# Kernel optimization log

Measured on AMD Instinct MI355X. Metric: run time of the kernel, lower is better.

Reference implementation:

```python
import jax, jax.numpy as jnp
import numpy as np

NEG = -9.0e15

def gat_layer(X, adj_mask, W, Wb, a1, a2, ab):
    # X: [N, Fin]; W: [Fin, Fout]; a1,a2: [Fout]; ab: scalar
    h = X @ W + Wb                                   # [N, Fout]
    # a([h_i || h_j]) = h_i@a1 + h_j@a2 + ab  (decomposition of concat+linear)
    e = jax.nn.leaky_relu((h @ a1)[:, None] + (h @ a2)[None, :] + ab,
                          negative_slope=0.2)        # [N, N]
    e = jnp.where(adj_mask, e, NEG)
    attn = jax.nn.softmax(e, axis=1)                 # [N, N]
    return jax.nn.elu(attn @ h)                      # [N, Fout]

def setup_inputs() -> dict:
    key = jax.random.key(0)
    ks = jax.random.split(key, 12)
    N, Fin, Fh, H, Fout = 4096, 512, 128, 4, 64
    X = jax.random.normal(ks[0], (N, Fin), dtype=jnp.float32)
    adjacency_matrix = jax.random.randint(ks[1], (N, N), 0, 2, dtype=jnp.int32)
    s_in = 1.0 / np.sqrt(Fin)
    s_a = 1.0 / np.sqrt(2 * Fh)
    W_h  = jax.random.uniform(ks[2], (H, Fin, Fh), jnp.float32, -s_in, s_in)
    b_h  = jax.random.uniform(ks[3], (H, Fh), jnp.float32, -s_in, s_in)
    a1_h = jax.random.uniform(ks[4], (H, Fh), jnp.float32, -s_a, s_a)
    a2_h = jax.random.uniform(ks[5], (H, Fh), jnp.float32, -s_a, s_a)
    ab_h = jax.random.uniform(ks[6], (H,), jnp.float32, -s_a, s_a)
    Fcat = H * Fh
    s_c = 1.0 / np.sqrt(Fcat)
    s_ao = 1.0 / np.sqrt(2 * Fout)
    W_o  = jax.random.uniform(ks[7], (Fcat, Fout), jnp.float32, -s_c, s_c)
    b_o  = jax.random.uniform(ks[8], (Fout,), jnp.float32, -s_c, s_c)
    a1_o = jax.random.uniform(ks[9], (Fout,), jnp.float32, -s_ao, s_ao)
    a2_o = jax.random.uniform(ks[10], (Fout,), jnp.float32, -s_ao, s_ao)
    ab_o = jax.random.uniform(ks[11], (), jnp.float32, -s_ao, s_ao)
    return {"X": X, "adjacency_matrix": adjacency_matrix,
            "W_h": W_h, "b_h": b_h, "a1_h": a1_h, "a2_h": a2_h, "ab_h": ab_h,
            "W_o": W_o, "b_o": b_o, "a1_o": a1_o, "a2_o": a2_o, "ab_o": ab_o}

def reference(X, adjacency_matrix, W_h, b_h, a1_h, a2_h, ab_h,
              W_o, b_o, a1_o, a2_o, ab_o):
    adj_mask = adjacency_matrix > 0
    # per-head attention layers, vmapped over heads
    heads = jax.vmap(gat_layer, in_axes=(None, None, 0, 0, 0, 0, 0))(
        X, adj_mask, W_h, b_h, a1_h, a2_h, ab_h)      # [H, N, Fh]
    H, N, Fh = heads.shape
    x = jnp.transpose(heads, (1, 0, 2)).reshape(N, H * Fh)  # concat along features
    x = gat_layer(x, adj_mask, W_o, b_o, a1_o, a2_o, ab_o)  # [N, Fout]
    return jax.nn.log_softmax(x, axis=1)
```

## Files before the change

### kernel.cpp

```cpp
#include <hip/hip_runtime.h>
#include <math.h>

#define NN 4096
#define LOG2E 1.44269504088896340736f

using f32x4  = __attribute__((ext_vector_type(4))) float;
using bf16x4 = __attribute__((ext_vector_type(4))) __bf16;
using bf16x8 = __attribute__((ext_vector_type(8))) __bf16;

#if __has_builtin(__builtin_amdgcn_exp2f)
#define EXP2(x) __builtin_amdgcn_exp2f(x)
#else
#define EXP2(x) __expf((x) * 0.6931471805599453f)
#endif

#define WAITVM4_BARRIER asm volatile("s_waitcnt vmcnt(4)\ns_barrier" ::: "memory")
#define WAITVM0_BARRIER asm volatile("s_waitcnt vmcnt(0)\ns_barrier" ::: "memory")

template<int FH>
__device__ __forceinline__ void stage_tile(const __bf16* __restrict__ hgp,
                                           __bf16* dst, int tid) {
#pragma unroll
    for (int it = 0; it < FH / 32; it++) {
        int c = tid + it * 256;
        int f = c >> 3, sl = c & 7;
        int g = sl ^ (f & 7);
        __builtin_amdgcn_global_load_lds(
            (const __attribute__((address_space(1))) void*)(hgp + (size_t)f * NN + g * 8),
            (__attribute__((address_space(3))) void*)(dst + (size_t)c * 8), 16, 0, 0);
    }
}

__device__ __forceinline__ void stage_g(const __bf16* __restrict__ base, int ldk,
                                        __bf16* dst, int tid) {
#pragma unroll
    for (int it = 0; it < 2; it++) {
        int c = tid + it * 256;
        int f = c >> 3, sl = c & 7;
        int g = sl ^ (f & 7);
        __builtin_amdgcn_global_load_lds(
            (const __attribute__((address_space(1))) void*)(base + (size_t)f * ldk + g * 8),
            (__attribute__((address_space(3))) void*)(dst + (size_t)c * 8), 16, 0, 0);
    }
}

__global__ void prep_kernel(const int* __restrict__ adj, unsigned long long* __restrict__ bits,
                            const float* __restrict__ W_h, const float* __restrict__ b_h,
                            const float* __restrict__ W_o,
                            __bf16* __restrict__ Bt1, float* __restrict__ biasp,
                            __bf16* __restrict__ Bt2,
                            const float* __restrict__ X, __bf16* __restrict__ Xb,
                            float* __restrict__ zeros) {
    const int b = blockIdx.x, t = threadIdx.x;
    if (b < 1024) {
        int idx = b * 256 + t;
        {
            int n = idx >> 9, k = idx & 511;
            int h = n >> 7, f = n & 127;
            Bt1[idx] = (__bf16)W_h[(size_t)h * 512 * 128 + k * 128 + f];
        }
        if (idx < 64 * 512) {
            int n = idx >> 9, k = idx & 511;
            Bt2[idx] = (__bf16)W_o[k * 64 + n];
        }
        if (idx < 512) biasp[idx] = b_h[idx];
        if (idx < (10 * NN) / 4)
            *(f32x4*)(zeros + (size_t)idx * 4) = (f32x4){0.f, 0.f, 0.f, 0.f};
    } else if (b < 3072) {
        int i = (b - 1024) * 256 + t;
        f32x4 v = *(const f32x4*)(X + (size_t)i * 4);
        bf16x4 o;
#pragma unroll
        for (int q = 0; q < 4; q++) o[q] = (__bf16)v[q];
        *(bf16x4*)(Xb + (size_t)i * 4) = o;
    } else {
        int wave = (b - 3072) * 4 + (t >> 6);
        int lane = t & 63;
        int g0 = wave * 16;
        for (int it = 0; it < 16; it++) {
            int gw = g0 + it;
            int v = adj[(size_t)gw * 64 + lane];
            unsigned long long m = __ballot(v > 0);
            if (lane == 0) bits[gw] = m;
        }
    }
}

__global__ __launch_bounds__(256) void gemm_fused_kernel(
    const __bf16* __restrict__ A, const __bf16* __restrict__ Bt,
    const float* __restrict__ bias,
    const float* __restrict__ a1, const float* __restrict__ a2,
    __bf16* __restrict__ Ht, float* __restrict__ s1, float* __restrict__ s2,
    int M, int N, int K)
{
    __shared__ __attribute__((aligned(16))) __bf16 As[3][64 * 64];
    __shared__ __attribute__((aligned(16))) __bf16 Bs[3][64 * 64];
    const int tid = threadIdx.x, w = tid >> 6, l = tid & 63, o = l >> 4, rl = l & 15;
    const int bm = blockIdx.y * 64, bn = blockIdx.x * 64;
    f32x4 acc[4] = {};
    stage_g(A + (size_t)bm * K, K, &As[0][0], tid);
    stage_g(Bt + (size_t)bn * K, K, &Bs[0][0], tid);
    stage_g(A + (size_t)bm * K + 64, K, &As[1][0], tid);
    stage_g(Bt + (size_t)bn * K + 64, K, &Bs[1][0], tid);
    const int KB = K / 64;
    int b = 0;
    for (int kb = 0; kb < KB; kb++) {
        if (kb + 1 < KB) { WAITVM4_BARRIER; }
        else             { WAITVM0_BARRIER; }
#pragma unroll
        for (int kt = 0; kt < 2; kt++) {
            int ra = w * 16 + rl;
            int cg = kt * 4 + o;
            bf16x8 af = *(const bf16x8*)(&As[b][(ra * 8 + (cg ^ (ra & 7))) * 8]);
#pragma unroll
            for (int nt = 0; nt < 4; nt++) {
                int rb = nt * 16 + rl;
                bf16x8 bfr = *(const bf16x8*)(&Bs[b][(rb * 8 + (cg ^ (rb & 7))) * 8]);
                acc[nt] = __builtin_amdgcn_mfma_f32_16x16x32_bf16(af, bfr, acc[nt], 0, 0, 0);
            }
        }
        if (kb + 2 < KB) {
            int b2 = b + 2; if (b2 >= 3) b2 -= 3;
            stage_g(A + (size_t)bm * K + (kb + 2) * 64, K, &As[b2][0], tid);
            stage_g(Bt + (size_t)bn * K + (kb + 2) * 64, K, &Bs[b2][0], tid);
        }
        if (++b == 3) b = 0;
    }
    const int head = bn >> 7;
    const int row_base = bm + w * 16 + o * 4;
    float p1[4] = {0.f, 0.f, 0.f, 0.f}, p2[4] = {0.f, 0.f, 0.f, 0.f};
#pragma unroll
    for (int nt = 0; nt < 4; nt++) {
        int col = bn + nt * 16 + rl;
        float bv = bias[col];
        float a1v = a1[col] * LOG2E, a2v = a2[col] * LOG2E;
        bf16x4 hv;
#pragma unroll
        for (int r4 = 0; r4 < 4; r4++) {
            float h = acc[nt][r4] + bv;
            hv[r4] = (__bf16)h;
            p1[r4] += h * a1v;
            p2[r4] += h * a2v;
        }
        *(bf16x4*)(Ht + (size_t)col * M + row_base) = hv;
    }
#pragma unroll
    for (int r4 = 0; r4 < 4; r4++)
#pragma unroll
        for (int off = 1; off < 16; off <<= 1) {
            p1[r4] += __shfl_xor(p1[r4], off, 64);
            p2[r4] += __shfl_xor(p2[r4], off, 64);
        }
    if (rl == 0)
#pragma unroll
        for (int r4 = 0; r4 < 4; r4++) {
            atomicAdd(&s1[(size_t)head * M + row_base + r4], p1[r4]);
            atomicAdd(&s2[(size_t)head * M + row_base + r4], p2[r4]);
        }
}

template<int FH, int JSPLIT>
__global__ __launch_bounds__(256, 4) void attn_kernel(
    const __bf16* __restrict__ Htg,
    const unsigned long long* __restrict__ adj_bits,
    const float* __restrict__ s1_all, const float* __restrict__ s2_all,
    const float* __restrict__ ab_all,
    __bf16* __restrict__ accp,
    float* __restrict__ lg,
    int ldo)
{
    constexpr int NJT = NN / 64 / JSPLIT;
    constexpr int NTL = FH / 16;
    const int head = blockIdx.y;
    const int js   = blockIdx.z;
    const int row0 = blockIdx.x * 64;
    const int jt0  = js * NJT;
    const int tid = threadIdx.x;
    const int w = tid >> 6, l = tid & 63, o = l >> 4, rl = l & 15;
    const int myrow = row0 + w * 16 + rl;

    __shared__ __attribute__((aligned(16))) __bf16 hbuf[2][FH * 64];

    const float* s2 = s2_all + (size_t)head * NN;
    const __bf16* hg = Htg + (size_t)head * FH * NN;
    const float s1r = s1_all[(size_t)head * NN + myrow] + ab_all[head] * LOG2E;
    const float u0 = s1r;
    const float v0 = 0.2f * s1r;
    float lacc = 0.f;
    f32x4 acc[NTL] = {};

    unsigned long long aw;
    f32x4 sA0, sB0, sA1, sB1;

    auto PLOAD = [&](int jt) {
        aw = adj_bits[(size_t)myrow * 64 + jt];
        const float* sp = s2 + jt * 64 + o * 8;
        sA0 = *(const f32x4*)(sp);       sB0 = *(const f32x4*)(sp + 4);
        sA1 = *(const f32x4*)(sp + 32);  sB1 = *(const f32x4*)(sp + 36);
    };
    auto PMATH = [&](bf16x8& f0, bf16x8& f1) {
        float ps = 0.f;
        {
            unsigned int mb = (unsigned int)(aw >> (o * 8)) & 0xFFu;
#pragma unroll
            for (int q = 0; q < 8; q++) {
                float s = (q < 4) ? sA0[q] : sB0[q - 4];
                float t = fmaxf(s + u0, fmaf(0.2f, s, v0));
                t = ((mb >> q) & 1u) ? t : -1.0e20f;
                float p = EXP2(t);
                f0[q] = (__bf16)p; ps += p;
            }
        }
        {
            unsigned int mb = (unsigned int)(aw >> (32 + o * 8)) & 0xFFu;
#pragma unroll
            for (int q = 0; q < 8; q++) {
                float s = (q < 4) ? sA1[q] : sB1[q - 4];
                float t = fmaxf(s + u0, fmaf(0.2f, s, v0));
                t = ((mb >> q) & 1u) ? t : -1.0e20f;
                float p = EXP2(t);
                f1[q] = (__bf16)p; ps += p;
            }
        }
        lacc += ps;
    };

    stage_tile<FH>(hg + (size_t)jt0 * 64, &hbuf[0][0], tid);
    PLOAD(jt0);
    bf16x8 fc0, fc1, fn0, fn1;
    PMATH(fc0, fc1);
    if (NJT > 1) PLOAD(jt0 + 1);

    for (int jl = 0; jl < NJT; jl++) {
        const int b = jl & 1;
        const int jt = jt0 + jl;
        __syncthreads();
        if (jl + 1 < NJT)
            stage_tile<FH>(hg + (size_t)(jt + 1) * 64, &hbuf[b ^ 1][0], tid);
        __builtin_amdgcn_s_setprio(1);
        if (jl + 1 < NJT) PMATH(fn0, fn1);
        if (jl + 2 < NJT) PLOAD(jt + 2);
#pragma unroll
        for (int ntl = 0; ntl < NTL; ntl++) {
            int f = ntl * 16 + rl;
            int s0 = o ^ (rl & 7);
            int s1 = (4 + o) ^ (rl & 7);
            bf16x8 b0 = *(const bf16x8*)(&hbuf[b][(f * 8 + s0) * 8]);
            bf16x8 b1 = *(const bf16x8*)(&hbuf[b][(f * 8 + s1) * 8]);
            acc[ntl] = __builtin_amdgcn_mfma_f32_16x16x32_bf16(fc0, b0, acc[ntl], 0, 0, 0);
            acc[ntl] = __builtin_amdgcn_mfma_f32_16x16x32_bf16(fc1, b1, acc[ntl], 0, 0, 0);
        }
        __builtin_amdgcn_s_setprio(0);
        if (jl + 1 < NJT) { fc0 = fn0; fc1 = fn1; }
    }
    lacc += __shfl_xor(lacc, 16, 64);
    lacc += __shfl_xor(lacc, 32, 64);
    if (l < 16) lg[((size_t)head * JSPLIT + js) * NN + row0 + w * 16 + l] = lacc;
#pragma unroll
    for (int ntl = 0; ntl < NTL; ntl++)
#pragma unroll
        for (int r4 = 0; r4 < 4; r4++) {
            int grow = row0 + w * 16 + o * 4 + r4;
            int gcol = head * FH + ntl * 16 + rl;
            accp[((size_t)js * NN + grow) * ldo + gcol] = (__bf16)acc[ntl][r4];
        }
}

__global__ void combine1_kernel(const __bf16* __restrict__ accp, const float* __restrict__ lg,
                                __bf16* __restrict__ outb) {
    int gid = blockIdx.x * 256 + threadIdx.x;
    int row = gid >> 7, c4 = (gid & 127) * 4;
    int head = c4 >> 7;
    float lsum = 0.f;
#pragma unroll
    for (int js = 0; js < 4; js++) lsum += lg[((size_t)head * 4 + js) * NN + row];
    float inv = lsum > 0.f ? 1.f / lsum : 0.f;
    float v[4] = {0.f, 0.f, 0.f, 0.f};
#pragma unroll
    for (int js = 0; js < 4; js++) {
        bf16x4 t = *(const bf16x4*)(accp + ((size_t)js * NN + row) * 512 + c4);
#pragma unroll
        for (int q = 0; q < 4; q++) v[q] += (float)t[q];
    }
    bf16x4 ob;
#pragma unroll
    for (int q = 0; q < 4; q++) {
        float x = v[q] * inv;
        x = x > 0.f ? x : __expf(x) - 1.f;
        ob[q] = (__bf16)x;
    }
    *(bf16x4*)(outb + (size_t)row * 512 + c4) = ob;
}

__global__ void combine2_kernel(const __bf16* __restrict__ accp, const float* __restrict__ lg,
                                float* __restrict__ out) {
    int row = (blockIdx.x * 256 + threadIdx.x) >> 6;
    int lane = threadIdx.x & 63;
    if (row >= NN) return;
    float lsum = 0.f, v = 0.f;
#pragma unroll
    for (int js = 0; js < 16; js++) {
        lsum += lg[(size_t)js * NN + row];
        v += (float)accp[((size_t)js * NN + row) * 64 + lane];
    }
    float inv = lsum > 0.f ? 1.f / lsum : 0.f;
    v *= inv;
    v = v > 0.f ? v : __expf(v) - 1.f;
    float m = v;
#pragma unroll
    for (int off = 1; off < 64; off <<= 1) m = fmaxf(m, __shfl_xor(m, off, 64));
    float ex = __expf(v - m);
    float s = ex;
#pragma unroll
    for (int off = 1; off < 64; off <<= 1) s += __shfl_xor(s, off, 64);
    out[(size_t)row * 64 + lane] = v - m - __logf(s);
}

extern "C" void kernel_launch(void* const* d_in, const int* in_sizes, int n_in,
                              void* d_out, int out_size, void* d_ws, size_t ws_size,
                              hipStream_t stream) {
    const float* X    = (const float*)d_in[0];
    const int*   adj  = (const int*)d_in[1];
    const float* W_h  = (const float*)d_in[2];
    const float* b_h  = (const float*)d_in[3];
    const float* a1_h = (const float*)d_in[4];
    const float* a2_h = (const float*)d_in[5];
    const float* ab_h = (const float*)d_in[6];
    const float* W_o  = (const float*)d_in[7];
    const float* b_o  = (const float*)d_in[8];
    const float* a1_o = (const float*)d_in[9];
    const float* a2_o = (const float*)d_in[10];
    const float* ab_o = (const float*)d_in[11];
    float* out = (float*)d_out;

    char* ws = (char*)d_ws;
    auto alloc = [&](size_t bytes) {
        char* p = ws; ws += (bytes + 255) & ~(size_t)255; return p;
    };
    unsigned long long* adj_bits = (unsigned long long*)alloc((size_t)NN * 64 * 8);
    __bf16* Bt1    = (__bf16*)alloc((size_t)512 * 512 * 2);
    float*  biasp  = (float*)alloc(512 * 4);
    __bf16* Bt2    = (__bf16*)alloc((size_t)64 * 512 * 2);
    __bf16* Xb     = (__bf16*)alloc((size_t)NN * 512 * 2);
    float*  s1h    = (float*)alloc((size_t)4 * NN * 4);
    float*  s2h    = (float*)alloc((size_t)4 * NN * 4);
    float*  s1o    = (float*)alloc((size_t)NN * 4);
    float*  s2o    = (float*)alloc((size_t)NN * 4);
    __bf16* Htg    = (__bf16*)alloc((size_t)512 * NN * 2);
    __bf16* accp1  = (__bf16*)alloc((size_t)4 * NN * 512 * 2);
    float*  lg1    = (float*)alloc((size_t)16 * NN * 4);
    __bf16* outhb  = (__bf16*)alloc((size_t)NN * 512 * 2);
    __bf16* Ht2    = (__bf16*)alloc((size_t)64 * NN * 2);
    __bf16* accp2  = (__bf16*)alloc((size_t)16 * NN * 64 * 2);
    float*  lg2    = (float*)alloc((size_t)16 * NN * 4);

    prep_kernel<<<7168, 256, 0, stream>>>(adj, adj_bits, W_h, b_h, W_o,
                                          Bt1, biasp, Bt2, X, Xb, s1h);
    gemm_fused_kernel<<<dim3(8, 64), 256, 0, stream>>>(
        Xb, Bt1, biasp, a1_h, a2_h, Htg, s1h, s2h, NN, 512, 512);
    attn_kernel<128, 4><<<dim3(NN / 64, 4, 4), 256, 0, stream>>>(
        Htg, adj_bits, s1h, s2h, ab_h, accp1, lg1, 512);
    combine1_kernel<<<(NN * 128) / 256, 256, 0, stream>>>(accp1, lg1, outhb);
    gemm_fused_kernel<<<dim3(1, 64), 256, 0, stream>>>(
        outhb, Bt2, b_o, a1_o, a2_o, Ht2, s1o, s2o, NN, 64, 512);
    attn_kernel<64, 16><<<dim3(NN / 64, 1, 16), 256, 0, stream>>>(
        Ht2, adj_bits, s1o, s2o, ab_o, accp2, lg2, 64);
    combine2_kernel<<<(NN * 64) / 256, 256, 0, stream>>>(accp2, lg2, out);
}
```

Before: 204.1 us.

## Move adjacency bitpacking into first GEMM launch as extra z-slice blocks

Adjacency bit-packing moves out of the prep kernel and into 512 extra blocks (blockIdx.z==1) of the first fused GEMM launch. That lets the memory-bound 64MB int adjacency read run alongside the compute-bound GEMM instead of serially in prep. Each of these waves now packs 128 words instead of 16, so fewer blocks do the work with longer loops. Separately, the s_setprio(1) in the attention kernel now comes after the softmax math and prefetch, so only the MFMA section runs at raised priority.

```diff
diff --git a/kernel.cpp b/kernel.cpp
--- a/kernel.cpp
+++ b/kernel.cpp
@@ -44,8 +44,7 @@
     }
 }
 
-__global__ void prep_kernel(const int* __restrict__ adj, unsigned long long* __restrict__ bits,
-                            const float* __restrict__ W_h, const float* __restrict__ b_h,
+__global__ void prep_kernel(const float* __restrict__ W_h, const float* __restrict__ b_h,
                             const float* __restrict__ W_o,
                             __bf16* __restrict__ Bt1, float* __restrict__ biasp,
                             __bf16* __restrict__ Bt2,
@@ -66,23 +65,13 @@
         if (idx < 512) biasp[idx] = b_h[idx];
         if (idx < (10 * NN) / 4)
             *(f32x4*)(zeros + (size_t)idx * 4) = (f32x4){0.f, 0.f, 0.f, 0.f};
-    } else if (b < 3072) {
+    } else {
         int i = (b - 1024) * 256 + t;
         f32x4 v = *(const f32x4*)(X + (size_t)i * 4);
         bf16x4 o;
 #pragma unroll
         for (int q = 0; q < 4; q++) o[q] = (__bf16)v[q];
         *(bf16x4*)(Xb + (size_t)i * 4) = o;
-    } else {
-        int wave = (b - 3072) * 4 + (t >> 6);
-        int lane = t & 63;
-        int g0 = wave * 16;
-        for (int it = 0; it < 16; it++) {
-            int gw = g0 + it;
-            int v = adj[(size_t)gw * 64 + lane];
-            unsigned long long m = __ballot(v > 0);
-            if (lane == 0) bits[gw] = m;
-        }
     }
 }
 
@@ -91,11 +80,23 @@
     const float* __restrict__ bias,
     const float* __restrict__ a1, const float* __restrict__ a2,
     __bf16* __restrict__ Ht, float* __restrict__ s1, float* __restrict__ s2,
+    const int* __restrict__ adj, unsigned long long* __restrict__ adj_bits,
     int M, int N, int K)
 {
     __shared__ __attribute__((aligned(16))) __bf16 As[3][64 * 64];
     __shared__ __attribute__((aligned(16))) __bf16 Bs[3][64 * 64];
     const int tid = threadIdx.x, w = tid >> 6, l = tid & 63, o = l >> 4, rl = l & 15;
+    if (blockIdx.z == 1) {
+        int bid = blockIdx.y * gridDim.x + blockIdx.x;
+        int wv = bid * 4 + w;
+        for (int it = 0; it < 128; it++) {
+            int gw = wv * 128 + it;
+            int v = adj[(size_t)gw * 64 + l];
+            unsigned long long m = __ballot(v > 0);
+            if (l == 0) adj_bits[gw] = m;
+        }
+        return;
+    }
     const int bm = blockIdx.y * 64, bn = blockIdx.x * 64;
     f32x4 acc[4] = {};
     stage_g(A + (size_t)bm * K, K, &As[0][0], tid);
@@ -237,9 +238,9 @@
         __syncthreads();
         if (jl + 1 < NJT)
             stage_tile<FH>(hg + (size_t)(jt + 1) * 64, &hbuf[b ^ 1][0], tid);
-        __builtin_amdgcn_s_setprio(1);
         if (jl + 1 < NJT) PMATH(fn0, fn1);
         if (jl + 2 < NJT) PLOAD(jt + 2);
+        __builtin_amdgcn_s_setprio(1);
 #pragma unroll
         for (int ntl = 0; ntl < NTL; ntl++) {
             int f = ntl * 16 + rl;
@@ -354,15 +355,14 @@
     __bf16* accp2  = (__bf16*)alloc((size_t)16 * NN * 64 * 2);
     float*  lg2    = (float*)alloc((size_t)16 * NN * 4);
 
-    prep_kernel<<<7168, 256, 0, stream>>>(adj, adj_bits, W_h, b_h, W_o,
-                                          Bt1, biasp, Bt2, X, Xb, s1h);
-    gemm_fused_kernel<<<dim3(8, 64), 256, 0, stream>>>(
-        Xb, Bt1, biasp, a1_h, a2_h, Htg, s1h, s2h, NN, 512, 512);
+    prep_kernel<<<3072, 256, 0, stream>>>(W_h, b_h, W_o, Bt1, biasp, Bt2, X, Xb, s1h);
+    gemm_fused_kernel<<<dim3(8, 64, 2), 256, 0, stream>>>(
+        Xb, Bt1, biasp, a1_h, a2_h, Htg, s1h, s2h, adj, adj_bits, NN, 512, 512);
     attn_kernel<128, 4><<<dim3(NN / 64, 4, 4), 256, 0, stream>>>(
         Htg, adj_bits, s1h, s2h, ab_h, accp1, lg1, 512);
     combine1_kernel<<<(NN * 128) / 256, 256, 0, stream>>>(accp1, lg1, outhb);
-    gemm_fused_kernel<<<dim3(1, 64), 256, 0, stream>>>(
-        outhb, Bt2, b_o, a1_o, a2_o, Ht2, s1o, s2o, NN, 64, 512);
+    gemm_fused_kernel<<<dim3(1, 64, 1), 256, 0, stream>>>(
+        outhb, Bt2, b_o, a1_o, a2_o, Ht2, s1o, s2o, adj, adj_bits, NN, 64, 512);
     attn_kernel<64, 16><<<dim3(NN / 64, 1, 16), 256, 0, stream>>>(
         Ht2, adj_bits, s1o, s2o, ab_o, accp2, lg2, 64);
     combine2_kernel<<<(NN * 64) / 256, 256, 0, stream>>>(accp2, lg2, out);
```

Result: slower. 247.9 us (+21.4%).

## Fuse head-combine normalization and ELU into second-layer GEMM A-operand staging

Applied to the files above, without the earlier changes.

Drops the separate combine1 kernel. The second-layer GEMM now builds its A tiles directly from the split attention partials: it sums the 4 splits, scales by the reciprocal softmax denominators cached in shared memory, applies ELU, and writes swizzled bf16 into LDS. This removes one launch and the write and re-read of the 4096x512 intermediate. In exchange, the fused path uses double buffering with synchronous register-staged loads and only 64 blocks, so load latency may sit exposed in that GEMM. It also moves the s_setprio raise in the attention loop to after the softmax math and prefetch issue.

```diff
diff --git a/kernel.cpp b/kernel.cpp
--- a/kernel.cpp
+++ b/kernel.cpp
@@ -86,45 +86,109 @@
     }
 }
 
+template<int FUSEA>
 __global__ __launch_bounds__(256) void gemm_fused_kernel(
     const __bf16* __restrict__ A, const __bf16* __restrict__ Bt,
     const float* __restrict__ bias,
     const float* __restrict__ a1, const float* __restrict__ a2,
     __bf16* __restrict__ Ht, float* __restrict__ s1, float* __restrict__ s2,
+    const __bf16* __restrict__ accp, const float* __restrict__ lgin,
     int M, int N, int K)
 {
-    __shared__ __attribute__((aligned(16))) __bf16 As[3][64 * 64];
-    __shared__ __attribute__((aligned(16))) __bf16 Bs[3][64 * 64];
+    constexpr int NB = FUSEA ? 2 : 3;
+    __shared__ __attribute__((aligned(16))) __bf16 As[NB][64 * 64];
+    __shared__ __attribute__((aligned(16))) __bf16 Bs[NB][64 * 64];
+    __shared__ float sinv[4][64];
     const int tid = threadIdx.x, w = tid >> 6, l = tid & 63, o = l >> 4, rl = l & 15;
     const int bm = blockIdx.y * 64, bn = blockIdx.x * 64;
     f32x4 acc[4] = {};
-    stage_g(A + (size_t)bm * K, K, &As[0][0], tid);
-    stage_g(Bt + (size_t)bn * K, K, &Bs[0][0], tid);
-    stage_g(A + (size_t)bm * K + 64, K, &As[1][0], tid);
-    stage_g(Bt + (size_t)bn * K + 64, K, &Bs[1][0], tid);
     const int KB = K / 64;
-    int b = 0;
-    for (int kb = 0; kb < KB; kb++) {
-        if (kb + 1 < KB) { WAITVM4_BARRIER; }
-        else             { WAITVM0_BARRIER; }
-#pragma unroll
-        for (int kt = 0; kt < 2; kt++) {
-            int ra = w * 16 + rl;
-            int cg = kt * 4 + o;
-            bf16x8 af = *(const bf16x8*)(&As[b][(ra * 8 + (cg ^ (ra & 7))) * 8]);
-#pragma unroll
-            for (int nt = 0; nt < 4; nt++) {
-                int rb = nt * 16 + rl;
-                bf16x8 bfr = *(const bf16x8*)(&Bs[b][(rb * 8 + (cg ^ (rb & 7))) * 8]);
-                acc[nt] = __builtin_amdgcn_mfma_f32_16x16x32_bf16(af, bfr, acc[nt], 0, 0, 0);
-            }
-        }
-        if (kb + 2 < KB) {
-            int b2 = b + 2; if (b2 >= 3) b2 -= 3;
-            stage_g(A + (size_t)bm * K + (kb + 2) * 64, K, &As[b2][0], tid);
-            stage_g(Bt + (size_t)bn * K + (kb + 2) * 64, K, &Bs[b2][0], tid);
-        }
-        if (++b == 3) b = 0;
+
+    auto stageA_fused = [&](int kb, __bf16* dst) {
+#pragma unroll
+        for (int it = 0; it < 2; it++) {
+            int c = tid + it * 256;
+            int f = c >> 3, sl = c & 7;
+            int row = bm + f;
+            int col = kb * 64 + sl * 8;
+            float inv = sinv[kb >> 1][f];
+            float vs[8] = {0.f, 0.f, 0.f, 0.f, 0.f, 0.f, 0.f, 0.f};
+#pragma unroll
+            for (int js = 0; js < 4; js++) {
+                bf16x8 t = *(const bf16x8*)(accp + ((size_t)js * NN + row) * 512 + col);
+#pragma unroll
+                for (int q = 0; q < 8; q++) vs[q] += (float)t[q];
+            }
+            bf16x8 ob;
+#pragma unroll
+            for (int q = 0; q < 8; q++) {
+                float x = vs[q] * inv;
+                x = x > 0.f ? x : __expf(x) - 1.f;
+                ob[q] = (__bf16)x;
+            }
+            *(bf16x8*)(dst + ((size_t)f * 8 + (sl ^ (f & 7))) * 8) = ob;
+        }
+    };
+
+    if constexpr (FUSEA) {
+        {
+            int h = tid >> 6, r = tid & 63;
+            float ls = 0.f;
+#pragma unroll
+            for (int js = 0; js < 4; js++) ls += lgin[((size_t)(h * 4 + js)) * NN + bm + r];
+            sinv[h][r] = ls > 0.f ? 1.f / ls : 0.f;
+        }
+        __syncthreads();
+        stageA_fused(0, &As[0][0]);
+        stage_g(Bt + (size_t)bn * K, K, &Bs[0][0], tid);
+        for (int kb = 0; kb < KB; kb++) {
+            int b = kb & 1;
+            __syncthreads();
+            if (kb + 1 < KB) {
+                stageA_fused(kb + 1, &As[b ^ 1][0]);
+                stage_g(Bt + (size_t)bn * K + (kb + 1) * 64, K, &Bs[b ^ 1][0], tid);
+            }
+#pragma unroll
+            for (int kt = 0; kt < 2; kt++) {
+                int ra = w * 16 + rl;
+                int cg = kt * 4 + o;
+                bf16x8 af = *(const bf16x8*)(&As[b][(ra * 8 + (cg ^ (ra & 7))) * 8]);
+#pragma unroll
+                for (int nt = 0; nt < 4; nt++) {
+                    int rb = nt * 16 + rl;
+                    bf16x8 bfr = *(const bf16x8*)(&Bs[b][(rb * 8 + (cg ^ (rb & 7))) * 8]);
+                    acc[nt] = __builtin_amdgcn_mfma_f32_16x16x32_bf16(af, bfr, acc[nt], 0, 0, 0);
+                }
+            }
+        }
+    } else {
+        stage_g(A + (size_t)bm * K, K, &As[0][0], tid);
+        stage_g(Bt + (size_t)bn * K, K, &Bs[0][0], tid);
+        stage_g(A + (size_t)bm * K + 64, K, &As[1][0], tid);
+        stage_g(Bt + (size_t)bn * K + 64, K, &Bs[1][0], tid);
+        int b = 0;
+        for (int kb = 0; kb < KB; kb++) {
+            if (kb + 1 < KB) { WAITVM4_BARRIER; }
+            else             { WAITVM0_BARRIER; }
+#pragma unroll
+            for (int kt = 0; kt < 2; kt++) {
+                int ra = w * 16 + rl;
+                int cg = kt * 4 + o;
+                bf16x8 af = *(const bf16x8*)(&As[b][(ra * 8 + (cg ^ (ra & 7))) * 8]);
+#pragma unroll
+                for (int nt = 0; nt < 4; nt++) {
+                    int rb = nt * 16 + rl;
+                    bf16x8 bfr = *(const bf16x8*)(&Bs[b][(rb * 8 + (cg ^ (rb & 7))) * 8]);
+                    acc[nt] = __builtin_amdgcn_mfma_f32_16x16x32_bf16(af, bfr, acc[nt], 0, 0, 0);
+                }
+            }
+            if (kb + 2 < KB) {
+                int b2 = b + 2; if (b2 >= 3) b2 -= 3;
+                stage_g(A + (size_t)bm * K + (kb + 2) * 64, K, &As[b2][0], tid);
+                stage_g(Bt + (size_t)bn * K + (kb + 2) * 64, K, &Bs[b2][0], tid);
+            }
+            if (++b == 3) b = 0;
+        }
     }
     const int head = bn >> 7;
     const int row_base = bm + w * 16 + o * 4;
@@ -237,9 +301,9 @@
         __syncthreads();
         if (jl + 1 < NJT)
             stage_tile<FH>(hg + (size_t)(jt + 1) * 64, &hbuf[b ^ 1][0], tid);
-        __builtin_amdgcn_s_setprio(1);
         if (jl + 1 < NJT) PMATH(fn0, fn1);
         if (jl + 2 < NJT) PLOAD(jt + 2);
+        __builtin_amdgcn_s_setprio(1);
 #pragma unroll
         for (int ntl = 0; ntl < NTL; ntl++) {
             int f = ntl * 16 + rl;
@@ -264,32 +328,6 @@
             int gcol = head * FH + ntl * 16 + rl;
             accp[((size_t)js * NN + grow) * ldo + gcol] = (__bf16)acc[ntl][r4];
         }
-}
-
-__global__ void combine1_kernel(const __bf16* __restrict__ accp, const float* __restrict__ lg,
-                                __bf16* __restrict__ outb) {
-    int gid = blockIdx.x * 256 + threadIdx.x;
-    int row = gid >> 7, c4 = (gid & 127) * 4;
-    int head = c4 >> 7;
-    float lsum = 0.f;
-#pragma unroll
-    for (int js = 0; js < 4; js++) lsum += lg[((size_t)head * 4 + js) * NN + row];
-    float inv = lsum > 0.f ? 1.f / lsum : 0.f;
-    float v[4] = {0.f, 0.f, 0.f, 0.f};
-#pragma unroll
-    for (int js = 0; js < 4; js++) {
-        bf16x4 t = *(const bf16x4*)(accp + ((size_t)js * NN + row) * 512 + c4);
-#pragma unroll
-        for (int q = 0; q < 4; q++) v[q] += (float)t[q];
-    }
-    bf16x4 ob;
-#pragma unroll
-    for (int q = 0; q < 4; q++) {
-        float x = v[q] * inv;
-        x = x > 0.f ? x : __expf(x) - 1.f;
-        ob[q] = (__bf16)x;
-    }
-    *(bf16x4*)(outb + (size_t)row * 512 + c4) = ob;
 }
 
 __global__ void combine2_kernel(const __bf16* __restrict__ accp, const float* __restrict__ lg,
@@ -349,20 +387,18 @@
     __bf16* Htg    = (__bf16*)alloc((size_t)512 * NN * 2);
     __bf16* accp1  = (__bf16*)alloc((size_t)4 * NN * 512 * 2);
     float*  lg1    = (float*)alloc((size_t)16 * NN * 4);
-    __bf16* outhb  = (__bf16*)alloc((size_t)NN * 512 * 2);
     __bf16* Ht2    = (__bf16*)alloc((size_t)64 * NN * 2);
     __bf16* accp2  = (__bf16*)alloc((size_t)16 * NN * 64 * 2);
     float*  lg2    = (float*)alloc((size_t)16 * NN * 4);
 
     prep_kernel<<<7168, 256, 0, stream>>>(adj, adj_bits, W_h, b_h, W_o,
                                           Bt1, biasp, Bt2, X, Xb, s1h);
-    gemm_fused_kernel<<<dim3(8, 64), 256, 0, stream>>>(
-        Xb, Bt1, biasp, a1_h, a2_h, Htg, s1h, s2h, NN, 512, 512);
+    gemm_fused_kernel<0><<<dim3(8, 64), 256, 0, stream>>>(
+        Xb, Bt1, biasp, a1_h, a2_h, Htg, s1h, s2h, nullptr, nullptr, NN, 512, 512);
     attn_kernel<128, 4><<<dim3(NN / 64, 4, 4), 256, 0, stream>>>(
         Htg, adj_bits, s1h, s2h, ab_h, accp1, lg1, 512);
-    combine1_kernel<<<(NN * 128) / 256, 256, 0, stream>>>(accp1, lg1, outhb);
-    gemm_fused_kernel<<<dim3(1, 64), 256, 0, stream>>>(
-        outhb, Bt2, b_o, a1_o, a2_o, Ht2, s1o, s2o, NN, 64, 512);
+    gemm_fused_kernel<1><<<dim3(1, 64), 256, 0, stream>>>(
+        nullptr, Bt2, b_o, a1_o, a2_o, Ht2, s1o, s2o, accp1, lg1, NN, 64, 512);
     attn_kernel<64, 16><<<dim3(NN / 64, 1, 16), 256, 0, stream>>>(
         Ht2, adj_bits, s1o, s2o, ab_o, accp2, lg2, 64);
     combine2_kernel<<<(NN * 64) / 256, 256, 0, stream>>>(accp2, lg2, out);
```

Measured after the change: 205.3 us. About the same (+0.6%).
